# Kernel optimization log

Hardware: AMD Instinct MI355X
Metric: run time of the kernel (lower is better)

## Reference

```python
import jax, jax.numpy as jnp
import numpy as np

BATCH = 32768
NUM_CLASSES = 1000

def setup_inputs() -> dict:
    key = jax.random.key(0)
    k1, k2 = jax.random.split(key)
    input = jax.random.normal(k1, (BATCH, NUM_CLASSES), dtype=jnp.float32)
    target = jax.random.randint(k2, (BATCH, NUM_CLASSES), 0, 2, dtype=jnp.int32)
    return {"input": input, "target": target}

def reference(input, target):
    # LSEP: loss = log(1 + sum_{i} sum_{p in pos_i} sum_{n in neg_i} exp(x[i,n] - x[i,p]))
    # The pair sum factorizes per sample:
    #   sum_{p,n} exp(x_n - x_p) = (sum_{n in neg} exp(x_n)) * (sum_{p in pos} exp(-x_p))
    pos = target > 0
    neg = target == 0
    s_neg = jnp.sum(jnp.where(neg, jnp.exp(input), 0.0), axis=1)   # [B]
    s_pos = jnp.sum(jnp.where(pos, jnp.exp(-input), 0.0), axis=1)  # [B]
    total = jnp.sum(s_neg * s_pos)
    return jnp.log1p(total).reshape(1).astype(jnp.float32)
```

## Files before the change

kernel.cpp:

```cpp
#include <hip/hip_runtime.h>
#include <math.h>

#define BATCH   32768
#define NCLS    1000
#define NC4     250
#define NBLOCKS 2048
#define NWAVES  (NBLOCKS * 4)
#define RPW     (BATCH / NWAVES)

__device__ __forceinline__ void acc4(float4 xv, int4 tv, float& sn, float& sp) {
    float e0 = __expf(tv.x == 0 ? xv.x : -xv.x);
    float e1 = __expf(tv.y == 0 ? xv.y : -xv.y);
    float e2 = __expf(tv.z == 0 ? xv.z : -xv.z);
    float e3 = __expf(tv.w == 0 ? xv.w : -xv.w);
    sn += (tv.x == 0) ? e0 : 0.0f;  sp += (tv.x == 0) ? 0.0f : e0;
    sn += (tv.y == 0) ? e1 : 0.0f;  sp += (tv.y == 0) ? 0.0f : e1;
    sn += (tv.z == 0) ? e2 : 0.0f;  sp += (tv.z == 0) ? 0.0f : e2;
    sn += (tv.w == 0) ? e3 : 0.0f;  sp += (tv.w == 0) ? 0.0f : e3;
}

__global__ __launch_bounds__(256, 4) void lsep_row_kernel(
    const float* __restrict__ x,
    const int*   __restrict__ t,
    float* __restrict__ wave_out) {

    const int tid   = threadIdx.x;
    const int lane  = tid & 63;
    const int gwave = blockIdx.x * 4 + (tid >> 6);

    const bool tail = (lane + 192 < NC4);

    const float4* xp = (const float4*)x + (size_t)gwave * NC4;
    const int4*   tp = (const int4*)t + (size_t)gwave * NC4;
    const size_t rstep = (size_t)NWAVES * NC4;

    float acc = 0.0f;

    #pragma unroll
    for (int pr = 0; pr < RPW / 2; ++pr) {
        const float4* xA = xp + (size_t)(2 * pr)     * rstep;
        const int4*   tA = tp + (size_t)(2 * pr)     * rstep;
        const float4* xB = xp + (size_t)(2 * pr + 1) * rstep;
        const int4*   tB = tp + (size_t)(2 * pr + 1) * rstep;

        float4 xa0, xa1, xa2, xa3, xb0, xb1, xb2, xb3;
        int4   ta0, ta1, ta2, ta3, tb0, tb1, tb2, tb3;

        xa0 = xA[lane];       ta0 = tA[lane];
        xb0 = xB[lane];       tb0 = tB[lane];
        xa1 = xA[lane + 64];  ta1 = tA[lane + 64];
        xb1 = xB[lane + 64];  tb1 = tB[lane + 64];
        xa2 = xA[lane + 128]; ta2 = tA[lane + 128];
        xb2 = xB[lane + 128]; tb2 = tB[lane + 128];
        if (tail) {
            xa3 = xA[lane + 192]; ta3 = tA[lane + 192];
            xb3 = xB[lane + 192]; tb3 = tB[lane + 192];
        }

        float snA = 0.0f, spA = 0.0f, snB = 0.0f, spB = 0.0f;
        acc4(xa0, ta0, snA, spA);
        acc4(xb0, tb0, snB, spB);
        acc4(xa1, ta1, snA, spA);
        acc4(xb1, tb1, snB, spB);
        acc4(xa2, ta2, snA, spA);
        acc4(xb2, tb2, snB, spB);
        if (tail) {
            acc4(xa3, ta3, snA, spA);
            acc4(xb3, tb3, snB, spB);
        }

        #pragma unroll
        for (int off = 32; off > 0; off >>= 1) {
            snA += __shfl_down(snA, off, 64);
            spA += __shfl_down(spA, off, 64);
            snB += __shfl_down(snB, off, 64);
            spB += __shfl_down(spB, off, 64);
        }

        if (lane == 0) acc += snA * spA + snB * spB;
    }

    if (lane == 0) wave_out[gwave] = acc;
}

__global__ __launch_bounds__(256) void lsep_reduce_kernel(
    const float* __restrict__ wave_out,
    float* __restrict__ out) {

    const int tid = threadIdx.x;
    const float4* r4 = (const float4*)wave_out;

    float4 a[8];
    #pragma unroll
    for (int j = 0; j < 8; ++j)
        a[j] = r4[tid + 256 * j];

    float v = 0.0f;
    #pragma unroll
    for (int j = 0; j < 8; ++j)
        v += (a[j].x + a[j].y) + (a[j].z + a[j].w);

    #pragma unroll
    for (int off = 32; off > 0; off >>= 1)
        v += __shfl_down(v, off, 64);

    __shared__ float sv[4];
    const int wave = tid >> 6;
    const int lane = tid & 63;
    if (lane == 0) sv[wave] = v;
    __syncthreads();

    if (tid == 0) {
        float total = (sv[0] + sv[1]) + (sv[2] + sv[3]);
        out[0] = log1pf(total);
    }
}

extern "C" void kernel_launch(void* const* d_in, const int* in_sizes, int n_in,
                              void* d_out, int out_size, void* d_ws, size_t ws_size,
                              hipStream_t stream) {
    const float* x = (const float*)d_in[0];
    const int*   t = (const int*)d_in[1];
    float* out     = (float*)d_out;
    float* wave_ws = (float*)d_ws;

    lsep_row_kernel<<<NBLOCKS, 256, 0, stream>>>(x, t, wave_ws);
    lsep_reduce_kernel<<<1, 256, 0, stream>>>(wave_ws, out);
}
```

Before: 269.9 us.

## Software-pipeline row loads with inline asm global loads and explicit vmcnt waits

Replaces the paired-row loop with a hand-pipelined schedule using inline-asm global_load_dwordx4 and s_waitcnt vmcnt, issuing the next row's loads while the current row is computed and reduced. The tail branch is replaced with a clamped column index and a zero weight so every lane issues the same loads without divergence. This keeps more memory requests in flight per wave to hide HBM latency. Risks: the inline asm hides the loads from the compiler's dependency tracking, the clamped tail loads add redundant traffic, and correctness depends on the hand-counted vmcnt values.

Result: no change. 268.3 us (-0.6%).

```diff
diff --git a/kernel.cpp b/kernel.cpp
--- a/kernel.cpp
+++ b/kernel.cpp
@@ -8,11 +8,20 @@
 #define NWAVES  (NBLOCKS * 4)
 #define RPW     (BATCH / NWAVES)
 
-__device__ __forceinline__ void acc4(float4 xv, int4 tv, float& sn, float& sp) {
-    float e0 = __expf(tv.x == 0 ? xv.x : -xv.x);
-    float e1 = __expf(tv.y == 0 ? xv.y : -xv.y);
-    float e2 = __expf(tv.z == 0 ? xv.z : -xv.z);
-    float e3 = __expf(tv.w == 0 ? xv.w : -xv.w);
+#define GLOAD4(dst, ptr) \
+    asm volatile("global_load_dwordx4 %0, %1, off" : "=v"(dst) : "v"(ptr) : "memory")
+
+#define WAITVM(N) do { \
+    asm volatile("s_waitcnt vmcnt(" #N ")" ::: "memory"); \
+    __builtin_amdgcn_sched_barrier(0); \
+} while (0)
+
+__device__ __forceinline__ void acc4w(float4 xv, int4 tv, float w,
+                                      float& sn, float& sp) {
+    float e0 = w * __expf(tv.x == 0 ? xv.x : -xv.x);
+    float e1 = w * __expf(tv.y == 0 ? xv.y : -xv.y);
+    float e2 = w * __expf(tv.z == 0 ? xv.z : -xv.z);
+    float e3 = w * __expf(tv.w == 0 ? xv.w : -xv.w);
     sn += (tv.x == 0) ? e0 : 0.0f;  sp += (tv.x == 0) ? 0.0f : e0;
     sn += (tv.y == 0) ? e1 : 0.0f;  sp += (tv.y == 0) ? 0.0f : e1;
     sn += (tv.z == 0) ? e2 : 0.0f;  sp += (tv.z == 0) ? 0.0f : e2;
@@ -28,59 +37,75 @@
     const int lane  = tid & 63;
     const int gwave = blockIdx.x * 4 + (tid >> 6);
 
-    const bool tail = (lane + 192 < NC4);
+    const int   cid3 = (lane < 58) ? (192 + lane) : 249;
+    const float w3   = (lane < 58) ? 1.0f : 0.0f;
 
+    const size_t rstep = (size_t)NWAVES * NC4;
     const float4* xp = (const float4*)x + (size_t)gwave * NC4;
     const int4*   tp = (const int4*)t + (size_t)gwave * NC4;
-    const size_t rstep = (size_t)NWAVES * NC4;
+
+    float4 xa0, xa1, xa2, xa3, xb0, xb1, xb2, xb3;
+    int4   ta0, ta1, ta2, ta3, tb0, tb1, tb2, tb3;
+
+    #define ISSUE_A(r) do { const float4* xr = xp + (size_t)(r) * rstep; \
+                            const int4*   tr = tp + (size_t)(r) * rstep; \
+        GLOAD4(xa0, xr + lane); GLOAD4(xa1, xr + 64 + lane); \
+        GLOAD4(xa2, xr + 128 + lane); GLOAD4(xa3, xr + cid3); \
+        GLOAD4(ta0, tr + lane); GLOAD4(ta1, tr + 64 + lane); \
+        GLOAD4(ta2, tr + 128 + lane); GLOAD4(ta3, tr + cid3); } while (0)
+    #define ISSUE_B(r) do { const float4* xr = xp + (size_t)(r) * rstep; \
+                            const int4*   tr = tp + (size_t)(r) * rstep; \
+        GLOAD4(xb0, xr + lane); GLOAD4(xb1, xr + 64 + lane); \
+        GLOAD4(xb2, xr + 128 + lane); GLOAD4(xb3, xr + cid3); \
+        GLOAD4(tb0, tr + lane); GLOAD4(tb1, tr + 64 + lane); \
+        GLOAD4(tb2, tr + 128 + lane); GLOAD4(tb3, tr + cid3); } while (0)
 
     float acc = 0.0f;
+    float sn, sp;
 
-    #pragma unroll
-    for (int pr = 0; pr < RPW / 2; ++pr) {
-        const float4* xA = xp + (size_t)(2 * pr)     * rstep;
-        const int4*   tA = tp + (size_t)(2 * pr)     * rstep;
-        const float4* xB = xp + (size_t)(2 * pr + 1) * rstep;
-        const int4*   tB = tp + (size_t)(2 * pr + 1) * rstep;
+    #define REDUCE() do { \
+        _Pragma("unroll") \
+        for (int off = 32; off > 0; off >>= 1) { \
+            sn += __shfl_down(sn, off, 64); \
+            sp += __shfl_down(sp, off, 64); \
+        } \
+        if (lane == 0) acc += sn * sp; \
+    } while (0)
 
-        float4 xa0, xa1, xa2, xa3, xb0, xb1, xb2, xb3;
-        int4   ta0, ta1, ta2, ta3, tb0, tb1, tb2, tb3;
+    ISSUE_A(0);
+    ISSUE_B(1);
 
-        xa0 = xA[lane];       ta0 = tA[lane];
-        xb0 = xB[lane];       tb0 = tB[lane];
-        xa1 = xA[lane + 64];  ta1 = tA[lane + 64];
-        xb1 = xB[lane + 64];  tb1 = tB[lane + 64];
-        xa2 = xA[lane + 128]; ta2 = tA[lane + 128];
-        xb2 = xB[lane + 128]; tb2 = tB[lane + 128];
-        if (tail) {
-            xa3 = xA[lane + 192]; ta3 = tA[lane + 192];
-            xb3 = xB[lane + 192]; tb3 = tB[lane + 192];
-        }
+    WAITVM(8);
+    sn = 0.f; sp = 0.f;
+    acc4w(xa0, ta0, 1.0f, sn, sp); acc4w(xa1, ta1, 1.0f, sn, sp);
+    acc4w(xa2, ta2, 1.0f, sn, sp); acc4w(xa3, ta3, w3,  sn, sp);
+    ISSUE_A(2);
+    REDUCE();
 
-        float snA = 0.0f, spA = 0.0f, snB = 0.0f, spB = 0.0f;
-        acc4(xa0, ta0, snA, spA);
-        acc4(xb0, tb0, snB, spB);
-        acc4(xa1, ta1, snA, spA);
-        acc4(xb1, tb1, snB, spB);
-        acc4(xa2, ta2, snA, spA);
-        acc4(xb2, tb2, snB, spB);
-        if (tail) {
-            acc4(xa3, ta3, snA, spA);
-            acc4(xb3, tb3, snB, spB);
-        }
+    WAITVM(8);
+    sn = 0.f; sp = 0.f;
+    acc4w(xb0, tb0, 1.0f, sn, sp); acc4w(xb1, tb1, 1.0f, sn, sp);
+    acc4w(xb2, tb2, 1.0f, sn, sp); acc4w(xb3, tb3, w3,  sn, sp);
+    ISSUE_B(3);
+    REDUCE();
 
-        #pragma unroll
-        for (int off = 32; off > 0; off >>= 1) {
-            snA += __shfl_down(snA, off, 64);
-            spA += __shfl_down(spA, off, 64);
-            snB += __shfl_down(snB, off, 64);
-            spB += __shfl_down(spB, off, 64);
-        }
+    WAITVM(8);
+    sn = 0.f; sp = 0.f;
+    acc4w(xa0, ta0, 1.0f, sn, sp); acc4w(xa1, ta1, 1.0f, sn, sp);
+    acc4w(xa2, ta2, 1.0f, sn, sp); acc4w(xa3, ta3, w3,  sn, sp);
+    REDUCE();
 
-        if (lane == 0) acc += snA * spA + snB * spB;
-    }
+    WAITVM(0);
+    sn = 0.f; sp = 0.f;
+    acc4w(xb0, tb0, 1.0f, sn, sp); acc4w(xb1, tb1, 1.0f, sn, sp);
+    acc4w(xb2, tb2, 1.0f, sn, sp); acc4w(xb3, tb3, w3,  sn, sp);
+    REDUCE();
 
     if (lane == 0) wave_out[gwave] = acc;
+
+    #undef ISSUE_A
+    #undef ISSUE_B
+    #undef REDUCE
 }
 
 __global__ __launch_bounds__(256) void lsep_reduce_kernel(
```
